# Kernel tuning notes

Measured on AMD Instinct MI355X. Metric: run time of the kernel, lower is better.

The kernel has to match this reference:

```python
import jax, jax.numpy as jnp
import numpy as np

B, N, K = 4, 100000, 128
Q_MIN = 0.5
S_B = 1.0
POT_SCALE = 1.0
REP_SCALE = 1.0
BETA_SCALE = 1.0
E_WEIGHT = 1.0
POS_WEIGHT = 1.0
TIME_WEIGHT = 1.0
HUBER_D = 2.0


def setup_inputs() -> dict:
    key = jax.random.key(0)
    ks = jax.random.split(key, 9)
    return {
        "beta": jax.random.uniform(ks[0], (B, N), dtype=jnp.float32),
        "ccoords": jax.random.normal(ks[1], (B, N, 2), dtype=jnp.float32),
        "pred_energy": jax.random.uniform(ks[2], (B, N), dtype=jnp.float32),
        "pred_pos": jax.random.normal(ks[3], (B, N, 2), dtype=jnp.float32),
        "pred_time": jax.random.uniform(ks[4], (B, N), dtype=jnp.float32),
        "t_energy": jax.random.uniform(ks[5], (B, N), dtype=jnp.float32),
        "t_pos": jax.random.normal(ks[6], (B, N, 2), dtype=jnp.float32),
        "t_time": jax.random.uniform(ks[7], (B, N), dtype=jnp.float32),
        "t_idx": jax.random.randint(ks[8], (B, N), 0, K + 1, dtype=jnp.int32),
    }


def _huber(x, d):
    a = jnp.abs(x)
    return jnp.where(a <= d, 0.5 * x * x, d * (a - 0.5 * d))


def _oc_loss(beta, ccoords, pred_energy, pred_pos, pred_time,
             t_energy, t_pos, t_time, t_idx):
    eps = 1e-4
    beta = jnp.clip(beta, eps, 1.0 - eps)
    q = jnp.arctanh(beta) ** 2 + Q_MIN                     # [B,N]

    obj = t_idx - 1                                        # -1 = noise, 0..K-1 = object id
    M = obj[:, :, None] == jnp.arange(K, dtype=jnp.int32)  # [B,N,K] bool membership
    Mf = M.astype(q.dtype)
    obj_exists = jnp.any(M, axis=1)                        # [B,K]
    exf = obj_exists.astype(q.dtype)

    # condensation point per object = member hit with max charge q (segment argmax)
    q_masked = jnp.where(M, q[:, :, None], -1.0)           # [B,N,K]
    alpha = jnp.argmax(q_masked, axis=1)                   # [B,K]
    x_alpha = jnp.take_along_axis(ccoords, alpha[:, :, None], axis=1)  # [B,K,2]
    q_alpha = jnp.take_along_axis(q, alpha, axis=1)        # [B,K]
    beta_alpha = jnp.take_along_axis(beta, alpha, axis=1)  # [B,K]

    # pairwise hit <-> condensation-point distances, [B,N,K]
    diff = ccoords[:, :, None, :] - x_alpha[:, None, :, :]
    dist = jnp.sqrt(jnp.sum(diff * diff, axis=-1) + 1e-12)

    qq = q[:, :, None] * q_alpha[:, None, :] * exf[:, None, :]
    v_att = qq * (dist * dist) * Mf
    v_rep = qq * jax.nn.relu(1.0 - dist) * (1.0 - Mf)
    n_tot = jnp.asarray(B * N, q.dtype)
    L_att = jnp.sum(v_att) / n_tot
    L_rep = jnp.sum(v_rep) / n_tot

    # beta loss: pull condensation-point betas to 1, suppress noise betas
    n_obj = jnp.maximum(jnp.sum(exf), 1.0)
    L_beta_obj = jnp.sum((1.0 - beta_alpha) * exf) / n_obj
    noise = (t_idx == 0).astype(q.dtype)
    L_noise = jnp.sum(beta * noise) / jnp.maximum(jnp.sum(noise), 1.0)
    L_beta = L_beta_obj + S_B * L_noise

    # payload losses, beta-weighted over non-noise hits
    p = (jnp.arctanh(beta) ** 2) * (1.0 - noise)           # [B,N]
    p_sum = jnp.maximum(jnp.sum(p), 1e-6)
    L_energy = jnp.sum(p * _huber(pred_energy - t_energy, HUBER_D)) / p_sum
    L_pos = jnp.sum(p * jnp.sum((pred_pos - t_pos) ** 2, axis=-1)) / p_sum
    L_time = jnp.sum(p * (pred_time - t_time) ** 2) / p_sum

    return (POT_SCALE * L_att + REP_SCALE * L_rep + BETA_SCALE * L_beta
            + E_WEIGHT * L_energy + POS_WEIGHT * L_pos + TIME_WEIGHT * L_time)


def reference(beta, ccoords, pred_energy, pred_pos, pred_time,
              t_energy, t_pos, t_time, t_idx):
    return _oc_loss(beta, ccoords, pred_energy, pred_pos, pred_time,
                    t_energy, t_pos, t_time, t_idx)
```

## Files before the change

### kernel.cpp

```cpp
#include <hip/hip_runtime.h>
#include <math.h>

#define BB 4
#define NN 100000
#define KK 128


__device__ __forceinline__ float clipb(float b) {
    const float eps = 1e-4f;
    return fminf(fmaxf(b, eps), 1.0f - eps);
}

__global__ void k_argmax(const float* __restrict__ beta,
                         const int* __restrict__ tidx,
                         unsigned long long* __restrict__ packed) {
    int b = blockIdx.y;
    __shared__ unsigned long long smax[KK];
    for (int t = threadIdx.x; t < KK; t += blockDim.x) smax[t] = 0ULL;
    __syncthreads();
    const float* betab = beta + b * NN;
    const int*   tib   = tidx + b * NN;
    for (int n = blockIdx.x * blockDim.x + threadIdx.x; n < NN;
         n += gridDim.x * blockDim.x) {
        int obj = tib[n] - 1;
        if (obj >= 0) {
            float bc = clipb(betab[n]);
            float at = atanhf(bc);
            float q  = at * at + 0.5f;
            unsigned long long key =
                ((unsigned long long)__float_as_uint(q) << 32) |
                (unsigned long long)(0xFFFFFFFFu - (unsigned)n);
            atomicMax(&smax[obj], key);
        }
    }
    __syncthreads();
    for (int t = threadIdx.x; t < KK; t += blockDim.x) {
        unsigned long long v = smax[t];
        if (v) atomicMax(&packed[b * KK + t], v);
    }
}

__global__ void k_gather(const unsigned long long* __restrict__ packed,
                         const float* __restrict__ beta,
                         const float2* __restrict__ cc,
                         float4* __restrict__ sobj,
                         float* __restrict__ acc) {
    int t = blockIdx.x * blockDim.x + threadIdx.x;
    if (t >= BB * KK) return;
    int b = t / KK;
    unsigned long long v = packed[t];
    float4 o = make_float4(0.f, 0.f, 0.f, 0.f);
    if (v) {
        unsigned n = 0xFFFFFFFFu - (unsigned)(v & 0xFFFFFFFFu);
        int idx = b * NN + (int)n;
        float qa = __uint_as_float((unsigned)(v >> 32));
        float ba = clipb(beta[idx]);
        float2 c = cc[idx];
        o.x = c.x; o.y = c.y; o.z = qa; o.w = 1.0f;
        atomicAdd(&acc[8], 1.0f);
        atomicAdd(&acc[9], 1.0f - ba);
    }
    sobj[t] = o;
}

__global__ void __launch_bounds__(256) k_main(
    const float*  __restrict__ beta, const float2* __restrict__ cc,
    const float*  __restrict__ pe,   const float2* __restrict__ pp,
    const float*  __restrict__ pt,   const float*  __restrict__ te,
    const float2* __restrict__ tp,   const float*  __restrict__ tt,
    const int*    __restrict__ tidx, const float4* __restrict__ sobjg,
    float* __restrict__ acc) {
    int b = blockIdx.y;
    __shared__ float4 sobj[KK];
    __shared__ float sred[4][8];
    for (int t = threadIdx.x; t < KK; t += blockDim.x) sobj[t] = sobjg[b * KK + t];
    __syncthreads();

    float p_att = 0.f, p_rep = 0.f, p_nb = 0.f, p_nc = 0.f;
    float p_ps = 0.f, p_e = 0.f, p_pos = 0.f, p_tm = 0.f;

    int n = blockIdx.x * blockDim.x + threadIdx.x;
    if (n < NN) {
        int idx = b * NN + n;
        float bc  = clipb(beta[idx]);
        float at  = atanhf(bc);
        float at2 = at * at;
        float q   = at2 + 0.5f;
        float2 c  = cc[idx];
        int ti    = tidx[idx];
        int obj   = ti - 1;

        float rep = 0.f;
        #pragma unroll 4
        for (int k = 0; k < KK; ++k) {
            float4 o = sobj[k];
            float dx = c.x - o.x, dy = c.y - o.y;
            float s = fmaf(dx, dx, fmaf(dy, dy, 1e-12f));
            float d = sqrtf(s);
            rep += o.z * fmaxf(1.0f - d, 0.0f);
        }
        if (obj >= 0) {
            float4 o = sobj[obj];
            float dx = c.x - o.x, dy = c.y - o.y;
            float s = fmaf(dx, dx, fmaf(dy, dy, 1e-12f));
            float d = sqrtf(s);
            rep   -= o.z * fmaxf(1.0f - d, 0.0f);
            p_att  = q * (o.z * (d * d));
        }
        p_rep = q * rep;

        if (ti == 0) {
            p_nb = bc;
            p_nc = 1.0f;
        } else {
            float p = at2;
            p_ps = p;
            float de = pe[idx] - te[idx];
            float a  = fabsf(de);
            float h  = (a <= 2.0f) ? (0.5f * de * de) : (2.0f * (a - 1.0f));
            p_e = p * h;
            float2 ppv = pp[idx], tpv = tp[idx];
            float dpx = ppv.x - tpv.x, dpy = ppv.y - tpv.y;
            p_pos = p * (dpx * dpx + dpy * dpy);
            float dt = pt[idx] - tt[idx];
            p_tm = p * dt * dt;
        }
    }

    float vals[8] = {p_att, p_rep, p_nb, p_nc, p_ps, p_e, p_pos, p_tm};
    int lane = threadIdx.x & 63, wave = threadIdx.x >> 6;
    #pragma unroll
    for (int i = 0; i < 8; ++i) {
        float v = vals[i];
        for (int off = 32; off > 0; off >>= 1) v += __shfl_down(v, off, 64);
        if (lane == 0) sred[wave][i] = v;
    }
    __syncthreads();
    if (threadIdx.x < 8) {
        float s = sred[0][threadIdx.x] + sred[1][threadIdx.x] +
                  sred[2][threadIdx.x] + sred[3][threadIdx.x];
        atomicAdd(&acc[threadIdx.x], s);
    }
}

__global__ void k_final(const float* __restrict__ acc, float* __restrict__ out) {
    float inv_n  = 1.0f / (float)(BB * NN);
    float L_att  = acc[0] * inv_n;
    float L_rep  = acc[1] * inv_n;
    float n_obj  = fmaxf(acc[8], 1.0f);
    float L_beta = acc[9] / n_obj + acc[2] / fmaxf(acc[3], 1.0f);
    float p_sum  = fmaxf(acc[4], 1e-6f);
    out[0] = L_att + L_rep + L_beta + (acc[5] + acc[6] + acc[7]) / p_sum;
}

extern "C" void kernel_launch(void* const* d_in, const int* in_sizes, int n_in,
                              void* d_out, int out_size, void* d_ws, size_t ws_size,
                              hipStream_t stream) {
    const float*  beta = (const float*)d_in[0];
    const float2* cc   = (const float2*)d_in[1];
    const float*  pe   = (const float*)d_in[2];
    const float2* pp   = (const float2*)d_in[3];
    const float*  pt   = (const float*)d_in[4];
    const float*  te   = (const float*)d_in[5];
    const float2* tp   = (const float2*)d_in[6];
    const float*  tt   = (const float*)d_in[7];
    const int*    ti   = (const int*)d_in[8];

    unsigned long long* packed = (unsigned long long*)d_ws;
    float4* sobj = (float4*)((char*)d_ws + 4096);
    float*  acc  = (float*)((char*)d_ws + 12288);
    float*  out  = (float*)d_out;

    hipMemsetAsync(packed, 0, 4096, stream);
    hipMemsetAsync(acc, 0, 64, stream);

    k_argmax<<<dim3(64, BB), 256, 0, stream>>>(beta, ti, packed);
    k_gather<<<dim3(2), 256, 0, stream>>>(packed, beta, cc, sobj, acc);
    k_main<<<dim3((NN + 255) / 256, BB), 256, 0, stream>>>(
        beta, cc, pe, pp, pt, te, tp, tt, ti, sobj, acc);
    k_final<<<1, 1, 0, stream>>>(acc, out);
}
```

Measured before the change: 130.5 us.

## Process two hits per thread, argmax on clipped beta, merge memsets

Measured after the change: 131.1 us. Within noise of the previous version (+0.4%).

```diff
diff --git a/kernel.cpp b/kernel.cpp
--- a/kernel.cpp
+++ b/kernel.cpp
@@ -7,8 +7,7 @@
 
 
 __device__ __forceinline__ float clipb(float b) {
-    const float eps = 1e-4f;
-    return fminf(fmaxf(b, eps), 1.0f - eps);
+    return fminf(fmaxf(b, 1e-4f), 1.0f - 1e-4f);
 }
 
 __global__ void k_argmax(const float* __restrict__ beta,
@@ -24,12 +23,9 @@
          n += gridDim.x * blockDim.x) {
         int obj = tib[n] - 1;
         if (obj >= 0) {
-            float bc = clipb(betab[n]);
-            float at = atanhf(bc);
-            float q  = at * at + 0.5f;
-            unsigned long long key =
-                ((unsigned long long)__float_as_uint(q) << 32) |
-                (unsigned long long)(0xFFFFFFFFu - (unsigned)n);
+            unsigned hi = __float_as_uint(clipb(betab[n]));
+            unsigned long long key = ((unsigned long long)hi << 32) |
+                                     (unsigned long long)(0xFFFFFFFFu - (unsigned)n);
             atomicMax(&smax[obj], key);
         }
     }
@@ -41,7 +37,6 @@
 }
 
 __global__ void k_gather(const unsigned long long* __restrict__ packed,
-                         const float* __restrict__ beta,
                          const float2* __restrict__ cc,
                          float4* __restrict__ sobj,
                          float* __restrict__ acc) {
@@ -52,16 +47,17 @@
     float4 o = make_float4(0.f, 0.f, 0.f, 0.f);
     if (v) {
         unsigned n = 0xFFFFFFFFu - (unsigned)(v & 0xFFFFFFFFu);
-        int idx = b * NN + (int)n;
-        float qa = __uint_as_float((unsigned)(v >> 32));
-        float ba = clipb(beta[idx]);
-        float2 c = cc[idx];
-        o.x = c.x; o.y = c.y; o.z = qa; o.w = 1.0f;
+        float ba = __uint_as_float((unsigned)(v >> 32));
+        float at = atanhf(ba);
+        float2 c = cc[b * NN + (int)n];
+        o.x = c.x; o.y = c.y; o.z = at * at + 0.5f; o.w = 1.0f;
         atomicAdd(&acc[8], 1.0f);
         atomicAdd(&acc[9], 1.0f - ba);
     }
     sobj[t] = o;
 }
+
+#define HH 2
 
 __global__ void __launch_bounds__(256) k_main(
     const float*  __restrict__ beta, const float2* __restrict__ cc,
@@ -79,51 +75,66 @@
     float p_att = 0.f, p_rep = 0.f, p_nb = 0.f, p_nc = 0.f;
     float p_ps = 0.f, p_e = 0.f, p_pos = 0.f, p_tm = 0.f;
 
-    int n = blockIdx.x * blockDim.x + threadIdx.x;
-    if (n < NN) {
-        int idx = b * NN + n;
+    int n0 = blockIdx.x * (256 * HH) + threadIdx.x;
+    int n1 = n0 + 256;
+    bool v0 = n0 < NN, v1 = n1 < NN;
+    int i0 = b * NN + (v0 ? n0 : 0);
+    int i1 = b * NN + (v1 ? n1 : 0);
+
+    float2 c0 = cc[i0], c1 = cc[i1];
+    float rep0 = 0.f, rep1 = 0.f;
+
+    #pragma unroll 8
+    for (int k = 0; k < KK; ++k) {
+        float4 o = sobj[k];
+        float dx0 = c0.x - o.x, dy0 = c0.y - o.y;
+        float dx1 = c1.x - o.x, dy1 = c1.y - o.y;
+        float s0 = fmaf(dx0, dx0, fmaf(dy0, dy0, 1e-12f));
+        float s1 = fmaf(dx1, dx1, fmaf(dy1, dy1, 1e-12f));
+        float d0 = sqrtf(s0), d1 = sqrtf(s1);
+        rep0 = fmaf(o.z, fmaxf(1.0f - d0, 0.0f), rep0);
+        rep1 = fmaf(o.z, fmaxf(1.0f - d1, 0.0f), rep1);
+    }
+
+    #pragma unroll
+    for (int h = 0; h < HH; ++h) {
+        bool  vld = h ? v1 : v0;
+        int   idx = h ? i1 : i0;
+        float rep = h ? rep1 : rep0;
+        float2 c  = h ? c1 : c0;
+        if (!vld) continue;
+
         float bc  = clipb(beta[idx]);
         float at  = atanhf(bc);
         float at2 = at * at;
         float q   = at2 + 0.5f;
-        float2 c  = cc[idx];
-        int ti    = tidx[idx];
-        int obj   = ti - 1;
+        int   ti  = tidx[idx];
+        int   obj = ti - 1;
 
-        float rep = 0.f;
-        #pragma unroll 4
-        for (int k = 0; k < KK; ++k) {
-            float4 o = sobj[k];
-            float dx = c.x - o.x, dy = c.y - o.y;
-            float s = fmaf(dx, dx, fmaf(dy, dy, 1e-12f));
-            float d = sqrtf(s);
-            rep += o.z * fmaxf(1.0f - d, 0.0f);
-        }
         if (obj >= 0) {
             float4 o = sobj[obj];
             float dx = c.x - o.x, dy = c.y - o.y;
             float s = fmaf(dx, dx, fmaf(dy, dy, 1e-12f));
             float d = sqrtf(s);
             rep   -= o.z * fmaxf(1.0f - d, 0.0f);
-            p_att  = q * (o.z * (d * d));
+            p_att += q * (o.z * s);
         }
-        p_rep = q * rep;
+        p_rep += q * rep;
 
         if (ti == 0) {
-            p_nb = bc;
-            p_nc = 1.0f;
+            p_nb += bc;
+            p_nc += 1.0f;
         } else {
-            float p = at2;
-            p_ps = p;
+            p_ps += at2;
             float de = pe[idx] - te[idx];
             float a  = fabsf(de);
-            float h  = (a <= 2.0f) ? (0.5f * de * de) : (2.0f * (a - 1.0f));
-            p_e = p * h;
+            float hb = (a <= 2.0f) ? (0.5f * de * de) : (2.0f * (a - 1.0f));
+            p_e  += at2 * hb;
             float2 ppv = pp[idx], tpv = tp[idx];
             float dpx = ppv.x - tpv.x, dpy = ppv.y - tpv.y;
-            p_pos = p * (dpx * dpx + dpy * dpy);
+            p_pos += at2 * (dpx * dpx + dpy * dpy);
             float dt = pt[idx] - tt[idx];
-            p_tm = p * dt * dt;
+            p_tm += at2 * dt * dt;
         }
     }
 
@@ -171,12 +182,11 @@
     float*  acc  = (float*)((char*)d_ws + 12288);
     float*  out  = (float*)d_out;
 
-    hipMemsetAsync(packed, 0, 4096, stream);
-    hipMemsetAsync(acc, 0, 64, stream);
+    hipMemsetAsync(d_ws, 0, 12352, stream);
 
     k_argmax<<<dim3(64, BB), 256, 0, stream>>>(beta, ti, packed);
-    k_gather<<<dim3(2), 256, 0, stream>>>(packed, beta, cc, sobj, acc);
-    k_main<<<dim3((NN + 255) / 256, BB), 256, 0, stream>>>(
+    k_gather<<<dim3(2), 256, 0, stream>>>(packed, cc, sobj, acc);
+    k_main<<<dim3((NN + 256 * HH - 1) / (256 * HH), BB), 256, 0, stream>>>(
         beta, cc, pe, pp, pt, te, tp, tt, ti, sobj, acc);
     k_final<<<1, 1, 0, stream>>>(acc, out);
 }
```
